# Performance work log

Measured on AMD Instinct MI355X. Metric: run time of the kernel, lower is better.

## Reference

```python
import jax, jax.numpy as jnp
import numpy as np

# ---- problem dims (match init_kwargs / input_specs) ----
MC = 2048        # max_concepts
D = 128          # embed_dim
B = 64           # batch
L = 16           # program length
NOBJ = 128       # objects per scene
FDIM = 512       # feature_dim
NN = MC + NOBJ   # num_nodes
TEMP = 3.0       # cosine temperature
TH = 0.8         # true_th (cosine, train==val)
POS = 10.0
NEG = -10.0
YES_IDX = 0      # protocol['concepts','yes']
NO_IDX = 1       # protocol['concepts','no']
INIT_VAR = 0.001


def setup_inputs() -> dict:
    key = jax.random.key(0)
    ks = jax.random.split(key, 6)
    scene = jax.random.normal(ks[0], (B, NOBJ, FDIM), jnp.float32)
    # program[:, :, 0] = op code in [0,7), program[:, :, 1] = argument index
    program = jax.random.randint(ks[1], (B, L, 2), 0, 7, dtype=jnp.int32)
    concept_table = jax.random.normal(ks[2], (MC, D), jnp.float32) * INIT_VAR
    relation_table = jax.random.normal(ks[3], (MC, D * D), jnp.float32) * INIT_VAR
    W_feat = jax.random.normal(ks[4], (FDIM, D), jnp.float32) * INIT_VAR
    b_feat = jax.random.normal(ks[5], (D,), jnp.float32) * INIT_VAR
    return {"scene": scene, "program": program, "concept_table": concept_table,
            "relation_table": relation_table, "W_feat": W_feat, "b_feat": b_feat}


def _cos_sim(x, y, eps=1e-8):
    # torch F.cosine_similarity semantics: clamp each norm at eps
    xn = jnp.maximum(jnp.linalg.norm(x, axis=-1), eps)
    yn = jnp.maximum(jnp.linalg.norm(y, axis=-1), eps)
    return jnp.sum(x * y, axis=-1) / (xn * yn)


def reference(scene, program, concept_table, relation_table, W_feat, b_feat):
    # feature_mlp (dim_hidden == 0 -> single Linear)
    objects = scene @ W_feat + b_feat                              # [B, NOBJ, D]
    # per-step embedded arguments
    concept_args = concept_table[program[:, :, 1]]                 # [B, L, D]
    rel_args = relation_table[program[:, :, 1]].reshape(B, L, D, D)
    node_is_concept = jnp.arange(NN) < MC                          # [NN]
    # all_nodes = concat(all_concepts, objects) per sample
    all_nodes = jnp.concatenate(
        [jnp.broadcast_to(concept_table[None], (B, MC, D)), objects], axis=1)  # [B, NN, D]

    def run_sample(nodes_i, ops_i, args_i, cargs_i, rargs_i):
        att0 = jnp.ones((NN,), jnp.float32)

        def body(att, inp):
            op, arg, cvec, rmat = inp

            def f_null(a):
                return a

            def f_sel_obj(a):  # select 'object_only': zero concept slots
                return jnp.where(node_is_concept, 0.0, a)

            def f_sel_con(a):  # select 'concept_only': zero object slots
                return jnp.where(node_is_concept, a, 0.0)

            def f_verify(a):
                sim = _cos_sim(nodes_i, cvec[None, :])             # [NN]
                return jnp.minimum(a, jax.nn.sigmoid((sim - TH) * TEMP))

            def f_choose(a):
                a = jnp.where(node_is_concept, 0.0, a)
                return a.at[arg].set(1.0)

            def f_exist(a):
                s = a.max()
                yes = s * POS
                no = POS - yes
                a = jnp.full_like(a, NEG)
                return a.at[YES_IDX].set(yes).at[NO_IDX].set(no)

            def f_transfer(a):
                gather = a @ nodes_i                               # [D]
                trans = gather @ rmat                              # [D]
                sim = _cos_sim(nodes_i, trans[None, :])            # [NN]
                return jax.nn.sigmoid((sim - TH) * TEMP) * a.max()

            new = jax.lax.switch(
                op, [f_null, f_sel_obj, f_sel_con, f_verify, f_choose,
                     f_exist, f_transfer], att)
            return new, new

        _, hist = jax.lax.scan(body, att0, (ops_i, args_i, cargs_i, rargs_i))
        return hist                                                # [L, NN]

    hist = jax.vmap(run_sample)(all_nodes, program[:, :, 0], program[:, :, 1],
                                concept_args, rel_args)            # [B, L, NN]
    attn_final = hist[:, -1, :MC]                                  # [B, MC]
    out = jax.nn.log_softmax(attn_final, axis=1)
    return out, hist
```

## Files before the change

kernel.cpp:

```cpp
#include <hip/hip_runtime.h>
#include <math.h>

#define MC   2048
#define DD   128
#define BB   64
#define LL   16
#define NOBJ 128
#define FDIM 512
#define NN   (MC + NOBJ)
#define TEMPC 3.0f
#define THC   0.8f
#define POSC  10.0f
#define NEGC  (-10.0f)
#define EPSC  1e-8f
#define NARG  8
#define NINF  (-3.402823466e38f)
#define NSCALE 256.0f

#define QB   4
#define PART (NN / QB)
#define TS   512
#define NEP  32

typedef unsigned short ushort_t;
typedef float v2f __attribute__((ext_vector_type(2)));

#if defined(__has_builtin)
#if __has_builtin(__builtin_amdgcn_cvt_pk_f32_fp8)
#define HAS_HW_FP8 1
#endif
#endif

__device__ __forceinline__ float e4m3_dec1(unsigned int bv) {
    unsigned int s = (bv >> 7) & 1u, E = (bv >> 3) & 15u, M = bv & 7u;
    float v;
    if (E) v = __uint_as_float(((E + 120u) << 23) | (M << 20));
    else   v = (float)M * 0.001953125f;
    return s ? -v : v;
}
__device__ __forceinline__ v2f f8pair_sw(unsigned int w) {
    v2f r; r[0] = e4m3_dec1(w & 0xffu); r[1] = e4m3_dec1((w >> 8) & 0xffu); return r;
}
#ifdef HAS_HW_FP8
#define F8LO(u) __builtin_amdgcn_cvt_pk_f32_fp8((u), false)
#define F8HI(u) __builtin_amdgcn_cvt_pk_f32_fp8((u), true)
#else
#define F8LO(u) f8pair_sw((u) & 0xffffu)
#define F8HI(u) f8pair_sw((u) >> 16)
#endif

__device__ __forceinline__ unsigned int f32_to_e4m3(float x) {
    float a = fabsf(x);
    unsigned int s = (__float_as_uint(x) >> 31) << 7;
    if (a == 0.0f) return s;
    if (a >= 448.0f) return s | 0x7Eu;
    int e; float m = frexpf(a, &e);
    if (e >= -5) {
        int mant = (int)rintf(m * 16.0f);
        if (mant == 16) { mant = 8; e++; if (e - 1 > 8) return s | 0x7Eu; }
        return s | ((unsigned)(e - 1 + 7) << 3) | (unsigned)(mant - 8);
    } else {
        int q = (int)rintf(a * 512.0f);
        if (q >= 8) return s | 0x08u;
        return s | (unsigned)q;
    }
}

#define DEC16(u, g) do { \
    v2f _p0 = F8LO((u).x), _p1 = F8HI((u).x), _p2 = F8LO((u).y), _p3 = F8HI((u).y); \
    v2f _p4 = F8LO((u).z), _p5 = F8HI((u).z), _p6 = F8LO((u).w), _p7 = F8HI((u).w); \
    g[0]=_p0[0]; g[1]=_p0[1]; g[2]=_p1[0];  g[3]=_p1[1]; \
    g[4]=_p2[0]; g[5]=_p2[1]; g[6]=_p3[0];  g[7]=_p3[1]; \
    g[8]=_p4[0]; g[9]=_p4[1]; g[10]=_p5[0]; g[11]=_p5[1]; \
    g[12]=_p6[0]; g[13]=_p6[1]; g[14]=_p7[0]; g[15]=_p7[1]; \
} while (0)

#define GEMB 256
#define CONB 512
#define SIGB 64

__global__ __launch_bounds__(256) void prep_all(
        const float* __restrict__ scene, const float* __restrict__ W,
        const float* __restrict__ bias, const float* __restrict__ ct,
        float* __restrict__ cnorm, float* __restrict__ onorm,
        unsigned char* __restrict__ ctf8, unsigned char* __restrict__ objf8,
        float* __restrict__ sigc, float* __restrict__ sigo,
        unsigned int* __restrict__ flags) {
    const int blk = blockIdx.x;
    const int tid = threadIdx.x;

    if (blk < GEMB) {
        __shared__ float sA[64][36];
        __shared__ float sB[64][132];
        __shared__ float cv[NARG][DD];
        __shared__ float cnn[NARG];
        const int b = blk >> 2, q3 = blk & 3;
        const int row0 = q3 * 32;
        if (blk == 0) {
            for (int i = tid; i < BB * NEP * QB; i += 256) flags[i] = 0u;
        }
        for (int i = tid; i < NARG * DD; i += 256) cv[i >> 7][i & 127] = ct[i];
        __syncthreads();
        if (tid < NARG) {
            float ss = 0.f;
            for (int i = 0; i < DD; i++) ss = fmaf(cv[tid][i], cv[tid][i], ss);
            cnn[tid] = fmaxf(sqrtf(ss), EPSC);
        }
        const int tx = tid & 31, ty = tid >> 5;
        float acc[4][4] = {{0.f,0.f,0.f,0.f},{0.f,0.f,0.f,0.f},{0.f,0.f,0.f,0.f},{0.f,0.f,0.f,0.f}};
        const float* sc = scene + ((size_t)b * NOBJ + row0) * FDIM;
        for (int k0 = 0; k0 < FDIM; k0 += 64) {
            {
                const int r = tid >> 3, kq = (tid & 7) * 8;
                const float* src = sc + (size_t)r * FDIM + k0 + kq;
                float4 v0 = *(const float4*)(src);
                float4 v1 = *(const float4*)(src + 4);
                sA[kq+0][r]=v0.x; sA[kq+1][r]=v0.y; sA[kq+2][r]=v0.z; sA[kq+3][r]=v0.w;
                sA[kq+4][r]=v1.x; sA[kq+5][r]=v1.y; sA[kq+6][r]=v1.z; sA[kq+7][r]=v1.w;
            }
            {
                const int kk = tid >> 2, colq = (tid & 3) * 32;
                const float* src = W + (size_t)(k0 + kk) * DD + colq;
                float4* dst = (float4*)&sB[kk][colq];
                #pragma unroll
                for (int j = 0; j < 8; j++) dst[j] = *(const float4*)(src + j * 4);
            }
            __syncthreads();
            #pragma unroll 8
            for (int kk = 0; kk < 64; kk++) {
                float4 a4 = *(const float4*)&sA[kk][ty * 4];
                float4 b4 = *(const float4*)&sB[kk][tx * 4];
                float av[4] = {a4.x, a4.y, a4.z, a4.w};
                float bv[4] = {b4.x, b4.y, b4.z, b4.w};
                #pragma unroll
                for (int i = 0; i < 4; i++)
                    #pragma unroll
                    for (int j = 0; j < 4; j++)
                        acc[i][j] = fmaf(av[i], bv[j], acc[i][j]);
            }
            __syncthreads();
        }
        {
            float4 bb4 = *(const float4*)(bias + tx * 4);
            float bv[4] = {bb4.x, bb4.y, bb4.z, bb4.w};
            #pragma unroll
            for (int i = 0; i < 4; i++)
                #pragma unroll
                for (int j = 0; j < 4; j++) acc[i][j] += bv[j];
        }
        float nrm4[4], inv4[4];
        #pragma unroll
        for (int i = 0; i < 4; i++) {
            float ss = 0.f;
            #pragma unroll
            for (int j = 0; j < 4; j++) ss = fmaf(acc[i][j], acc[i][j], ss);
            ss += __shfl_xor(ss, 1, 32);  ss += __shfl_xor(ss, 2, 32);
            ss += __shfl_xor(ss, 4, 32);  ss += __shfl_xor(ss, 8, 32);
            ss += __shfl_xor(ss, 16, 32);
            nrm4[i] = fmaxf(sqrtf(ss), EPSC);
            inv4[i] = NSCALE / nrm4[i];
        }
        const int grow = b * NOBJ + row0 + ty * 4;
        #pragma unroll
        for (int i = 0; i < 4; i++) {
            unsigned int w = f32_to_e4m3(acc[i][0] * inv4[i])
                           | (f32_to_e4m3(acc[i][1] * inv4[i]) << 8)
                           | (f32_to_e4m3(acc[i][2] * inv4[i]) << 16)
                           | (f32_to_e4m3(acc[i][3] * inv4[i]) << 24);
            *(unsigned int*)(objf8 + (size_t)(grow + i) * DD + tx * 4) = w;
        }
        if (tx == 0) {
            #pragma unroll
            for (int i = 0; i < 4; i++) onorm[grow + i] = nrm4[i];
        }
        #pragma unroll
        for (int a = 0; a < NARG; a++) {
            float dp[4];
            #pragma unroll
            for (int i = 0; i < 4; i++) {
                float d = 0.f;
                d = fmaf(acc[i][0], cv[a][tx*4+0], d);
                d = fmaf(acc[i][1], cv[a][tx*4+1], d);
                d = fmaf(acc[i][2], cv[a][tx*4+2], d);
                d = fmaf(acc[i][3], cv[a][tx*4+3], d);
                d += __shfl_xor(d, 1, 32);  d += __shfl_xor(d, 2, 32);
                d += __shfl_xor(d, 4, 32);  d += __shfl_xor(d, 8, 32);
                d += __shfl_xor(d, 16, 32);
                dp[i] = d;
            }
            if (tx == 0) {
                #pragma unroll
                for (int i = 0; i < 4; i++) {
                    float sim = dp[i] / (nrm4[i] * cnn[a]);
                    float g = 1.f / (1.f + __expf(-(sim - THC) * TEMPC));
                    sigo[((size_t)b * NARG + a) * NOBJ + row0 + ty * 4 + i] = g;
                }
            }
        }
        return;
    }

    if (blk < GEMB + CONB) {
        const int wid = tid >> 6, lane = tid & 63;
        const int r = (blk - GEMB) * 4 + wid;
        const float* row = ct + (size_t)r * DD;
        float2 xy = *(const float2*)(row + lane * 2);
        float ss = xy.x * xy.x + xy.y * xy.y;
        #pragma unroll
        for (int off = 32; off; off >>= 1) ss += __shfl_xor(ss, off, 64);
        float nrm = fmaxf(sqrtf(ss), EPSC);
        float inv = NSCALE / nrm;
        unsigned int b0 = f32_to_e4m3(xy.x * inv);
        unsigned int b1 = f32_to_e4m3(xy.y * inv);
        *(ushort_t*)(ctf8 + (size_t)r * DD + lane * 2) = (ushort_t)(b0 | (b1 << 8));
        if (lane == 0) cnorm[r] = nrm;
        return;
    }

    __shared__ float cv2[NARG][DD];
    __shared__ float cn2[NARG];
    for (int a = 0; a < NARG; a++)
        for (int i = tid; i < DD; i += 256) cv2[a][i] = ct[(size_t)a * DD + i];
    __syncthreads();
    if (tid < NARG) {
        float ss = 0.f;
        for (int i = 0; i < DD; i++) ss = fmaf(cv2[tid][i], cv2[tid][i], ss);
        cn2[tid] = fmaxf(sqrtf(ss), EPSC);
    }
    __syncthreads();
    const int sub = tid & 7, slot = tid >> 3;
    const int r = (blk - GEMB - CONB) * 32 + slot;
    const float* row = ct + (size_t)r * DD;
    float4 r0 = *(const float4*)(row + sub * 16 + 0);
    float4 r1 = *(const float4*)(row + sub * 16 + 4);
    float4 r2 = *(const float4*)(row + sub * 16 + 8);
    float4 r3 = *(const float4*)(row + sub * 16 + 12);
    float ssr = 0.f;
    ssr = fmaf(r0.x, r0.x, ssr); ssr = fmaf(r0.y, r0.y, ssr);
    ssr = fmaf(r0.z, r0.z, ssr); ssr = fmaf(r0.w, r0.w, ssr);
    ssr = fmaf(r1.x, r1.x, ssr); ssr = fmaf(r1.y, r1.y, ssr);
    ssr = fmaf(r1.z, r1.z, ssr); ssr = fmaf(r1.w, r1.w, ssr);
    ssr = fmaf(r2.x, r2.x, ssr); ssr = fmaf(r2.y, r2.y, ssr);
    ssr = fmaf(r2.z, r2.z, ssr); ssr = fmaf(r2.w, r2.w, ssr);
    ssr = fmaf(r3.x, r3.x, ssr); ssr = fmaf(r3.y, r3.y, ssr);
    ssr = fmaf(r3.z, r3.z, ssr); ssr = fmaf(r3.w, r3.w, ssr);
    ssr += __shfl_xor(ssr, 1, 64);
    ssr += __shfl_xor(ssr, 2, 64);
    ssr += __shfl_xor(ssr, 4, 64);
    float rn = fmaxf(sqrtf(ssr), EPSC);
    for (int a = 0; a < NARG; a++) {
        const float* c = &cv2[a][sub * 16];
        float dp = 0.f;
        dp = fmaf(r0.x, c[0], dp);  dp = fmaf(r0.y, c[1], dp);
        dp = fmaf(r0.z, c[2], dp);  dp = fmaf(r0.w, c[3], dp);
        dp = fmaf(r1.x, c[4], dp);  dp = fmaf(r1.y, c[5], dp);
        dp = fmaf(r1.z, c[6], dp);  dp = fmaf(r1.w, c[7], dp);
        dp = fmaf(r2.x, c[8], dp);  dp = fmaf(r2.y, c[9], dp);
        dp = fmaf(r2.z, c[10], dp); dp = fmaf(r2.w, c[11], dp);
        dp = fmaf(r3.x, c[12], dp); dp = fmaf(r3.y, c[13], dp);
        dp = fmaf(r3.z, c[14], dp); dp = fmaf(r3.w, c[15], dp);
        dp += __shfl_xor(dp, 1, 64);
        dp += __shfl_xor(dp, 2, 64);
        dp += __shfl_xor(dp, 4, 64);
        if (sub == 0) {
            float sim = dp / (rn * cn2[a]);
            float g = 1.f / (1.f + __expf(-(sim - THC) * TEMPC));
            sigc[(size_t)a * MC + r] = g;
        }
    }
}


#define GATH_ROW(row_) do { \
    const int _r = (row_); \
    uint4 _u = *(const uint4*)&nd[_r * DD + ((sub ^ (_r & 7)) << 4)]; \
    const float _a = att[_r] * nrmL[_r]; \
    float _g[16]; DEC16(_u, _g); \
    _Pragma("unroll") \
    for (int _j = 0; _j < 16; _j++) ac[_j] = fmaf(_a, _g[_j], ac[_j]); \
} while (0)

#define SIM_ROW(row_, COMB) do { \
    const int _r = (row_); \
    uint4 _u = *(const uint4*)&nd[_r * DD + ((sub ^ (_r & 7)) << 4)]; \
    float _g[16]; DEC16(_u, _g); \
    float _dp = 0.f; \
    _Pragma("unroll") \
    for (int _j = 0; _j < 16; _j++) _dp = fmaf(_g[_j], vv[_j], _dp); \
    _dp += __shfl_xor(_dp, 1, 64); \
    _dp += __shfl_xor(_dp, 2, 64); \
    _dp += __shfl_xor(_dp, 4, 64); \
    if (sub == 0) { \
        const float _sim = _dp * invden; \
        const float sg = 1.f / (1.f + __expf(-(_sim - THC) * TEMPC)); \
        COMB; \
    } \
} while (0)

#define AST(p, v) __hip_atomic_store((p), (v), __ATOMIC_RELAXED, __HIP_MEMORY_SCOPE_AGENT)
#define ALD(p)    __hip_atomic_load((p), __ATOMIC_RELAXED, __HIP_MEMORY_SCOPE_AGENT)

#define QBARRIER() do { \
    __syncthreads(); \
    if (tid == 0) { \
        unsigned int* _fl = myflag + (int)epoch * QB; \
        AST(&_fl[q], 1u); \
        unsigned _s; \
        do { _s = ALD(&_fl[0]) + ALD(&_fl[1]) + ALD(&_fl[2]) + ALD(&_fl[3]); } while (_s < 4u); \
    } \
    __syncthreads(); \
} while (0)

__global__ __launch_bounds__(TS) void scan_exec(
        const float* __restrict__ ct, const float* __restrict__ rt,
        const int* __restrict__ program,
        const float* __restrict__ cnorm, const float* __restrict__ onorm,
        const float* __restrict__ sigc, const float* __restrict__ sigo,
        const unsigned char* __restrict__ ctf8, const unsigned char* __restrict__ objf8,
        float* __restrict__ gpart, unsigned int* __restrict__ flags,
        float* __restrict__ out, float* __restrict__ hist) {

    const int b    = blockIdx.x & (BB - 1);
    const int q    = blockIdx.x >> 6;
    const int base = q * PART;
    const int tid  = threadIdx.x;
    const int lane = tid & 63, wid = tid >> 6;
    const int rg   = tid >> 3, sub = tid & 7;

    __shared__ __align__(16) unsigned char nd[PART * DD];
    __shared__ __align__(16) float att[PART];
    __shared__ __align__(16) float nrmL[PART];
    __shared__ __align__(16) float vec[DD];
    __shared__ __align__(16) float gvf[DD];
    __shared__ __align__(16) float part[8 * DD];
    __shared__ float wred[8];
    __shared__ float red2[8];
    __shared__ float s_sh;
    __shared__ float s_sh2;
    __shared__ int   sprog[2 * LL];

    const unsigned char* myobjf8 = objf8 + (size_t)b * NOBJ * DD;

    for (int idx = tid; idx < PART * 8; idx += TS) {
        const int row = idx >> 3, j = idx & 7;
        const int g   = base + row;
        const unsigned char* src = (g < MC) ? (ctf8 + (size_t)g * DD)
                                            : (myobjf8 + (size_t)(g - MC) * DD);
        uint4 v = *(const uint4*)(src + j * 16);
        *(uint4*)&nd[row * DD + ((j ^ (row & 7)) << 4)] = v;
    }
    for (int i = tid; i < PART; i += TS) {
        const int g = base + i;
        att[i]  = 1.0f;
        nrmL[i] = (g < MC) ? cnorm[g] : onorm[b * NOBJ + (g - MC)];
    }
    if (tid < 2 * LL) sprog[tid] = program[b * 2 * LL + tid];
    __syncthreads();

    unsigned int epoch = 0;
    float* gpb = gpart + (size_t)b * (2 * QB * 132);
    unsigned int* myflag = flags + b * (NEP * QB);

    for (int step = 0; step < LL; step++) {
        const int op  = sprog[2 * step];
        const int arg = sprog[2 * step + 1];
        float* hrow = hist + ((size_t)b * LL + step) * NN;

        if (op == 0) {
            for (int i = tid; i < PART; i += TS) hrow[base + i] = att[i];
        } else if (op == 1) {
            for (int i = tid; i < PART; i += TS) {
                const int g = base + i;
                const float nv = (g < MC) ? 0.0f : att[i];
                att[i] = nv; hrow[g] = nv;
            }
        } else if (op == 2) {
            for (int i = tid; i < PART; i += TS) {
                const int g = base + i;
                const float nv = (g < MC) ? att[i] : 0.0f;
                att[i] = nv; hrow[g] = nv;
            }
        } else if (op == 3 && arg < NARG) {
            const float* sc = sigc + (size_t)arg * MC;
            const float* so = sigo + ((size_t)b * NARG + arg) * NOBJ;
            for (int i = tid; i < PART; i += TS) {
                const int g = base + i;
                const float gg = (g < MC) ? sc[g] : so[g - MC];
                const float nv = fminf(att[i], gg);
                att[i] = nv; hrow[g] = nv;
            }
        } else if (op == 3) {
            __syncthreads();
            if (tid < DD) vec[tid] = ct[(size_t)arg * DD + tid];
            __syncthreads();
            const float cn = fmaxf(cnorm[arg], EPSC);
            const float invden = 1.0f / (NSCALE * cn);
            float vv[16];
            {
                const float4 v0 = *(const float4*)&vec[sub * 16 + 0];
                const float4 v1 = *(const float4*)&vec[sub * 16 + 4];
                const float4 v2 = *(const float4*)&vec[sub * 16 + 8];
                const float4 v3 = *(const float4*)&vec[sub * 16 + 12];
                vv[0]=v0.x; vv[1]=v0.y; vv[2]=v0.z; vv[3]=v0.w;
                vv[4]=v1.x; vv[5]=v1.y; vv[6]=v1.z; vv[7]=v1.w;
                vv[8]=v2.x; vv[9]=v2.y; vv[10]=v2.z; vv[11]=v2.w;
                vv[12]=v3.x; vv[13]=v3.y; vv[14]=v3.z; vv[15]=v3.w;
            }
            #pragma unroll
            for (int p = 0; p < 8; p++)
                SIM_ROW(rg + p * 64, { const float nv = fminf(att[_r], sg); att[_r] = nv; hrow[base + _r] = nv; });
            if (rg < PART - 512)
                SIM_ROW(rg + 512, { const float nv = fminf(att[_r], sg); att[_r] = nv; hrow[base + _r] = nv; });
            __syncthreads();
        } else if (op == 4) {
            for (int i = tid; i < PART; i += TS) {
                const int g = base + i;
                const float nv = (g < MC) ? ((g == arg) ? 1.0f : 0.0f) : att[i];
                att[i] = nv; hrow[g] = nv;
            }
        } else if (op == 5) {
            __syncthreads();
            float lm = NINF;
            for (int i = tid; i < PART; i += TS) lm = fmaxf(lm, att[i]);
            #pragma unroll
            for (int off = 32; off; off >>= 1) lm = fmaxf(lm, __shfl_xor(lm, off, 64));
            if (lane == 0) wred[wid] = lm;
            __syncthreads();
            epoch++;
            if (tid == 0) {
                float m = wred[0];
                #pragma unroll
                for (int w = 1; w < 8; w++) m = fmaxf(m, wred[w]);
                AST(&gpb[(size_t)((epoch & 1) * QB + q) * 132 + DD], m);
            }
            QBARRIER();
            if (tid == 0) {
                float* slotR = gpb + (size_t)((epoch & 1) * QB) * 132;
                float m = NINF;
                #pragma unroll
                for (int k = 0; k < QB; k++)
                    m = fmaxf(m, ALD(&slotR[k * 132 + DD]));
                s_sh = m;
            }
            __syncthreads();
            const float s = s_sh;
            const float yes = s * POSC, no = POSC - yes;
            for (int i = tid; i < PART; i += TS) {
                const int g = base + i;
                const float nv = (g == 0) ? yes : ((g == 1) ? no : NEGC);
                att[i] = nv; hrow[g] = nv;
            }
        } else if (op == 6) {
            __syncthreads();
            const float* rm = rt + (size_t)arg * (DD * DD);
            const int half = lane >> 5, dq = (lane & 31) * 4;
            float4 rmr[8];
            #pragma unroll
            for (int j = 0; j < 8; j++) {
                const int d = wid * 16 + half * 8 + j;
                rmr[j] = *(const float4*)(rm + (size_t)d * DD + dq);
            }
            float lm = NINF;
            for (int i = tid; i < PART; i += TS) lm = fmaxf(lm, att[i]);
            #pragma unroll
            for (int off = 32; off; off >>= 1) lm = fmaxf(lm, __shfl_xor(lm, off, 64));
            if (lane == 0) wred[wid] = lm;
            float ac[16];
            #pragma unroll
            for (int j = 0; j < 16; j++) ac[j] = 0.f;
            #pragma unroll
            for (int p = 0; p < 8; p++) GATH_ROW(rg + p * 64);
            if (rg < PART - 512) GATH_ROW(rg + 512);
            #pragma unroll
            for (int j = 0; j < 16; j++) {
                ac[j] += __shfl_xor(ac[j], 8, 64);
                ac[j] += __shfl_xor(ac[j], 16, 64);
                ac[j] += __shfl_xor(ac[j], 32, 64);
            }
            if (lane < 8) {
                float* dst = &part[wid * DD + lane * 16];
                #pragma unroll
                for (int k = 0; k < 4; k++)
                    *(float4*)(dst + k * 4) = make_float4(ac[k*4], ac[k*4+1], ac[k*4+2], ac[k*4+3]);
            }
            __syncthreads();
            epoch++;
            {
                float* slotW = gpb + (size_t)((epoch & 1) * QB + q) * 132;
                if (tid < DD) {
                    float gsum = 0.f;
                    #pragma unroll
                    for (int w = 0; w < 8; w++) gsum += part[w * DD + tid];
                    AST(&slotW[tid], gsum);
                }
                if (tid == DD) {
                    float m = wred[0];
                    #pragma unroll
                    for (int w = 1; w < 8; w++) m = fmaxf(m, wred[w]);
                    AST(&slotW[DD], m);
                }
            }
            QBARRIER();
            {
                float* slotR = gpb + (size_t)((epoch & 1) * QB) * 132;
                if (tid < DD) {
                    float gsum = 0.f;
                    #pragma unroll
                    for (int k = 0; k < QB; k++)
                        gsum += ALD(&slotR[k * 132 + tid]);
                    gvf[tid] = gsum;
                }
                if (tid == DD) {
                    float m = NINF;
                    #pragma unroll
                    for (int k = 0; k < QB; k++)
                        m = fmaxf(m, ALD(&slotR[k * 132 + DD]));
                    s_sh = m;
                }
            }
            __syncthreads();
            float qx = 0.f, qy = 0.f, qz = 0.f, qw = 0.f;
            #pragma unroll
            for (int j = 0; j < 8; j++) {
                const int d = wid * 16 + half * 8 + j;
                const float g = gvf[d];
                qx = fmaf(g, rmr[j].x, qx); qy = fmaf(g, rmr[j].y, qy);
                qz = fmaf(g, rmr[j].z, qz); qw = fmaf(g, rmr[j].w, qw);
            }
            qx += __shfl_xor(qx, 32, 64); qy += __shfl_xor(qy, 32, 64);
            qz += __shfl_xor(qz, 32, 64); qw += __shfl_xor(qw, 32, 64);
            if (lane < 32) *(float4*)&part[wid * DD + dq] = make_float4(qx, qy, qz, qw);
            __syncthreads();
            if (tid < DD) {
                float t = 0.f;
                #pragma unroll
                for (int w = 0; w < 8; w++) t += part[w * DD + tid];
                vec[tid] = t;
                float ss = t * t;
                #pragma unroll
                for (int off = 32; off; off >>= 1) ss += __shfl_xor(ss, off, 64);
                if (lane == 0) red2[wid] = ss;
            }
            __syncthreads();
            const float tn = fmaxf(sqrtf(red2[0] + red2[1]), EPSC * NSCALE);
            const float invden = 1.0f / (NSCALE * tn);
            const float s = s_sh;
            float vv[16];
            {
                const float4 v0 = *(const float4*)&vec[sub * 16 + 0];
                const float4 v1 = *(const float4*)&vec[sub * 16 + 4];
                const float4 v2 = *(const float4*)&vec[sub * 16 + 8];
                const float4 v3 = *(const float4*)&vec[sub * 16 + 12];
                vv[0]=v0.x; vv[1]=v0.y; vv[2]=v0.z; vv[3]=v0.w;
                vv[4]=v1.x; vv[5]=v1.y; vv[6]=v1.z; vv[7]=v1.w;
                vv[8]=v2.x; vv[9]=v2.y; vv[10]=v2.z; vv[11]=v2.w;
                vv[12]=v3.x; vv[13]=v3.y; vv[14]=v3.z; vv[15]=v3.w;
            }
            #pragma unroll
            for (int p = 0; p < 8; p++)
                SIM_ROW(rg + p * 64, { const float nv = sg * s; att[_r] = nv; hrow[base + _r] = nv; });
            if (rg < PART - 512)
                SIM_ROW(rg + 512, { const float nv = sg * s; att[_r] = nv; hrow[base + _r] = nv; });
            __syncthreads();
        }

        __syncthreads();
    }

    const int crows = (base + PART <= MC) ? PART : (MC - base);
    {
        float lm = NINF;
        for (int i = tid; i < crows; i += TS) lm = fmaxf(lm, att[i]);
        #pragma unroll
        for (int off = 32; off; off >>= 1) lm = fmaxf(lm, __shfl_xor(lm, off, 64));
        if (lane == 0) wred[wid] = lm;
    }
    __syncthreads();
    float mloc = wred[0];
    #pragma unroll
    for (int w = 1; w < 8; w++) mloc = fmaxf(mloc, wred[w]);
    {
        float lse = 0.f;
        for (int i = tid; i < crows; i += TS) lse += expf(att[i] - mloc);
        #pragma unroll
        for (int off = 32; off; off >>= 1) lse += __shfl_xor(lse, off, 64);
        if (lane == 0) red2[wid] = lse;
    }
    __syncthreads();
    epoch++;
    if (tid == 0) {
        float sloc = 0.f;
        #pragma unroll
        for (int w = 0; w < 8; w++) sloc += red2[w];
        float* slotW = gpb + (size_t)((epoch & 1) * QB + q) * 132;
        AST(&slotW[DD], mloc);
        AST(&slotW[DD + 1], sloc);
    }
    QBARRIER();
    if (tid == 0) {
        float* slotR = gpb + (size_t)((epoch & 1) * QB) * 132;
        float mg = NINF;
        float mq[QB], sq[QB];
        #pragma unroll
        for (int k = 0; k < QB; k++) {
            mq[k] = ALD(&slotR[k * 132 + DD]);
            sq[k] = ALD(&slotR[k * 132 + DD + 1]);
            mg = fmaxf(mg, mq[k]);
        }
        float se = 0.f;
        #pragma unroll
        for (int k = 0; k < QB; k++) se += sq[k] * expf(mq[k] - mg);
        s_sh  = mg;
        s_sh2 = logf(se);
    }
    __syncthreads();
    const float mglob = s_sh, ls = s_sh2;
    for (int i = tid; i < crows; i += TS)
        out[(size_t)b * MC + base + i] = att[i] - mglob - ls;
}

extern "C" void kernel_launch(void* const* d_in, const int* in_sizes, int n_in,
                              void* d_out, int out_size, void* d_ws, size_t ws_size,
                              hipStream_t stream) {
    const float* scene = (const float*)d_in[0];
    const int*   prog  = (const int*)d_in[1];
    const float* ct    = (const float*)d_in[2];
    const float* rt    = (const float*)d_in[3];
    const float* W     = (const float*)d_in[4];
    const float* bias  = (const float*)d_in[5];

    float* out  = (float*)d_out;
    float* hist = out + (size_t)BB * MC;

    float* cnorm = (float*)d_ws;
    float* onorm = cnorm + MC;
    float* sigc  = onorm + (size_t)BB * NOBJ;
    float* sigo  = sigc + (size_t)NARG * MC;
    float* gpart = sigo + (size_t)BB * NARG * NOBJ;
    unsigned int* flagbuf = (unsigned int*)(gpart + (size_t)BB * 2 * QB * 132);
    unsigned char* ctf8  = (unsigned char*)(flagbuf + BB * NEP * QB);
    unsigned char* objf8 = ctf8 + (size_t)MC * DD;

    prep_all<<<dim3(GEMB + CONB + SIGB), 256, 0, stream>>>(
        scene, W, bias, ct, cnorm, onorm, ctf8, objf8, sigc, sigo, flagbuf);
    scan_exec<<<dim3(BB * QB), TS, 0, stream>>>(ct, rt, prog, cnorm, onorm, sigc, sigo,
                                                ctf8, objf8, gpart, flagbuf, out, hist);
}
```

Measured before the change: 261.5 us.

## Fuse prep kernel into scan kernel, recomputing concept FP8/norms/sigmoids per block

Removes the separate prep_all launch and folds the object-feature GEMM, concept FP8 quantization, norms, and verify sigmoids into the scan kernel's prologue. Half the threads run the object GEMM while the other half quantize concept rows. Object data is exchanged across the four quarter-blocks of each sample through global memory and the existing flag barrier. The flag buffer is now cleared with a memset. This drops one kernel launch and the global round trip of precomputed concept data, but each of the 64 samples now recomputes the concept-table preprocessing redundantly. It also adds an extra inter-block barrier and raises shared-memory use per block.

```diff
diff --git a/kernel.cpp b/kernel.cpp
--- a/kernel.cpp
+++ b/kernel.cpp
@@ -21,6 +21,7 @@
 #define PART (NN / QB)
 #define TS   512
 #define NEP  32
+#define CTAIL 336
 
 typedef unsigned short ushort_t;
 typedef float v2f __attribute__((ext_vector_type(2)));
@@ -75,202 +76,6 @@
     g[12]=_p6[0]; g[13]=_p6[1]; g[14]=_p7[0]; g[15]=_p7[1]; \
 } while (0)
 
-#define GEMB 256
-#define CONB 512
-#define SIGB 64
-
-__global__ __launch_bounds__(256) void prep_all(
-        const float* __restrict__ scene, const float* __restrict__ W,
-        const float* __restrict__ bias, const float* __restrict__ ct,
-        float* __restrict__ cnorm, float* __restrict__ onorm,
-        unsigned char* __restrict__ ctf8, unsigned char* __restrict__ objf8,
-        float* __restrict__ sigc, float* __restrict__ sigo,
-        unsigned int* __restrict__ flags) {
-    const int blk = blockIdx.x;
-    const int tid = threadIdx.x;
-
-    if (blk < GEMB) {
-        __shared__ float sA[64][36];
-        __shared__ float sB[64][132];
-        __shared__ float cv[NARG][DD];
-        __shared__ float cnn[NARG];
-        const int b = blk >> 2, q3 = blk & 3;
-        const int row0 = q3 * 32;
-        if (blk == 0) {
-            for (int i = tid; i < BB * NEP * QB; i += 256) flags[i] = 0u;
-        }
-        for (int i = tid; i < NARG * DD; i += 256) cv[i >> 7][i & 127] = ct[i];
-        __syncthreads();
-        if (tid < NARG) {
-            float ss = 0.f;
-            for (int i = 0; i < DD; i++) ss = fmaf(cv[tid][i], cv[tid][i], ss);
-            cnn[tid] = fmaxf(sqrtf(ss), EPSC);
-        }
-        const int tx = tid & 31, ty = tid >> 5;
-        float acc[4][4] = {{0.f,0.f,0.f,0.f},{0.f,0.f,0.f,0.f},{0.f,0.f,0.f,0.f},{0.f,0.f,0.f,0.f}};
-        const float* sc = scene + ((size_t)b * NOBJ + row0) * FDIM;
-        for (int k0 = 0; k0 < FDIM; k0 += 64) {
-            {
-                const int r = tid >> 3, kq = (tid & 7) * 8;
-                const float* src = sc + (size_t)r * FDIM + k0 + kq;
-                float4 v0 = *(const float4*)(src);
-                float4 v1 = *(const float4*)(src + 4);
-                sA[kq+0][r]=v0.x; sA[kq+1][r]=v0.y; sA[kq+2][r]=v0.z; sA[kq+3][r]=v0.w;
-                sA[kq+4][r]=v1.x; sA[kq+5][r]=v1.y; sA[kq+6][r]=v1.z; sA[kq+7][r]=v1.w;
-            }
-            {
-                const int kk = tid >> 2, colq = (tid & 3) * 32;
-                const float* src = W + (size_t)(k0 + kk) * DD + colq;
-                float4* dst = (float4*)&sB[kk][colq];
-                #pragma unroll
-                for (int j = 0; j < 8; j++) dst[j] = *(const float4*)(src + j * 4);
-            }
-            __syncthreads();
-            #pragma unroll 8
-            for (int kk = 0; kk < 64; kk++) {
-                float4 a4 = *(const float4*)&sA[kk][ty * 4];
-                float4 b4 = *(const float4*)&sB[kk][tx * 4];
-                float av[4] = {a4.x, a4.y, a4.z, a4.w};
-                float bv[4] = {b4.x, b4.y, b4.z, b4.w};
-                #pragma unroll
-                for (int i = 0; i < 4; i++)
-                    #pragma unroll
-                    for (int j = 0; j < 4; j++)
-                        acc[i][j] = fmaf(av[i], bv[j], acc[i][j]);
-            }
-            __syncthreads();
-        }
-        {
-            float4 bb4 = *(const float4*)(bias + tx * 4);
-            float bv[4] = {bb4.x, bb4.y, bb4.z, bb4.w};
-            #pragma unroll
-            for (int i = 0; i < 4; i++)
-                #pragma unroll
-                for (int j = 0; j < 4; j++) acc[i][j] += bv[j];
-        }
-        float nrm4[4], inv4[4];
-        #pragma unroll
-        for (int i = 0; i < 4; i++) {
-            float ss = 0.f;
-            #pragma unroll
-            for (int j = 0; j < 4; j++) ss = fmaf(acc[i][j], acc[i][j], ss);
-            ss += __shfl_xor(ss, 1, 32);  ss += __shfl_xor(ss, 2, 32);
-            ss += __shfl_xor(ss, 4, 32);  ss += __shfl_xor(ss, 8, 32);
-            ss += __shfl_xor(ss, 16, 32);
-            nrm4[i] = fmaxf(sqrtf(ss), EPSC);
-            inv4[i] = NSCALE / nrm4[i];
-        }
-        const int grow = b * NOBJ + row0 + ty * 4;
-        #pragma unroll
-        for (int i = 0; i < 4; i++) {
-            unsigned int w = f32_to_e4m3(acc[i][0] * inv4[i])
-                           | (f32_to_e4m3(acc[i][1] * inv4[i]) << 8)
-                           | (f32_to_e4m3(acc[i][2] * inv4[i]) << 16)
-                           | (f32_to_e4m3(acc[i][3] * inv4[i]) << 24);
-            *(unsigned int*)(objf8 + (size_t)(grow + i) * DD + tx * 4) = w;
-        }
-        if (tx == 0) {
-            #pragma unroll
-            for (int i = 0; i < 4; i++) onorm[grow + i] = nrm4[i];
-        }
-        #pragma unroll
-        for (int a = 0; a < NARG; a++) {
-            float dp[4];
-            #pragma unroll
-            for (int i = 0; i < 4; i++) {
-                float d = 0.f;
-                d = fmaf(acc[i][0], cv[a][tx*4+0], d);
-                d = fmaf(acc[i][1], cv[a][tx*4+1], d);
-                d = fmaf(acc[i][2], cv[a][tx*4+2], d);
-                d = fmaf(acc[i][3], cv[a][tx*4+3], d);
-                d += __shfl_xor(d, 1, 32);  d += __shfl_xor(d, 2, 32);
-                d += __shfl_xor(d, 4, 32);  d += __shfl_xor(d, 8, 32);
-                d += __shfl_xor(d, 16, 32);
-                dp[i] = d;
-            }
-            if (tx == 0) {
-                #pragma unroll
-                for (int i = 0; i < 4; i++) {
-                    float sim = dp[i] / (nrm4[i] * cnn[a]);
-                    float g = 1.f / (1.f + __expf(-(sim - THC) * TEMPC));
-                    sigo[((size_t)b * NARG + a) * NOBJ + row0 + ty * 4 + i] = g;
-                }
-            }
-        }
-        return;
-    }
-
-    if (blk < GEMB + CONB) {
-        const int wid = tid >> 6, lane = tid & 63;
-        const int r = (blk - GEMB) * 4 + wid;
-        const float* row = ct + (size_t)r * DD;
-        float2 xy = *(const float2*)(row + lane * 2);
-        float ss = xy.x * xy.x + xy.y * xy.y;
-        #pragma unroll
-        for (int off = 32; off; off >>= 1) ss += __shfl_xor(ss, off, 64);
-        float nrm = fmaxf(sqrtf(ss), EPSC);
-        float inv = NSCALE / nrm;
-        unsigned int b0 = f32_to_e4m3(xy.x * inv);
-        unsigned int b1 = f32_to_e4m3(xy.y * inv);
-        *(ushort_t*)(ctf8 + (size_t)r * DD + lane * 2) = (ushort_t)(b0 | (b1 << 8));
-        if (lane == 0) cnorm[r] = nrm;
-        return;
-    }
-
-    __shared__ float cv2[NARG][DD];
-    __shared__ float cn2[NARG];
-    for (int a = 0; a < NARG; a++)
-        for (int i = tid; i < DD; i += 256) cv2[a][i] = ct[(size_t)a * DD + i];
-    __syncthreads();
-    if (tid < NARG) {
-        float ss = 0.f;
-        for (int i = 0; i < DD; i++) ss = fmaf(cv2[tid][i], cv2[tid][i], ss);
-        cn2[tid] = fmaxf(sqrtf(ss), EPSC);
-    }
-    __syncthreads();
-    const int sub = tid & 7, slot = tid >> 3;
-    const int r = (blk - GEMB - CONB) * 32 + slot;
-    const float* row = ct + (size_t)r * DD;
-    float4 r0 = *(const float4*)(row + sub * 16 + 0);
-    float4 r1 = *(const float4*)(row + sub * 16 + 4);
-    float4 r2 = *(const float4*)(row + sub * 16 + 8);
-    float4 r3 = *(const float4*)(row + sub * 16 + 12);
-    float ssr = 0.f;
-    ssr = fmaf(r0.x, r0.x, ssr); ssr = fmaf(r0.y, r0.y, ssr);
-    ssr = fmaf(r0.z, r0.z, ssr); ssr = fmaf(r0.w, r0.w, ssr);
-    ssr = fmaf(r1.x, r1.x, ssr); ssr = fmaf(r1.y, r1.y, ssr);
-    ssr = fmaf(r1.z, r1.z, ssr); ssr = fmaf(r1.w, r1.w, ssr);
-    ssr = fmaf(r2.x, r2.x, ssr); ssr = fmaf(r2.y, r2.y, ssr);
-    ssr = fmaf(r2.z, r2.z, ssr); ssr = fmaf(r2.w, r2.w, ssr);
-    ssr = fmaf(r3.x, r3.x, ssr); ssr = fmaf(r3.y, r3.y, ssr);
-    ssr = fmaf(r3.z, r3.z, ssr); ssr = fmaf(r3.w, r3.w, ssr);
-    ssr += __shfl_xor(ssr, 1, 64);
-    ssr += __shfl_xor(ssr, 2, 64);
-    ssr += __shfl_xor(ssr, 4, 64);
-    float rn = fmaxf(sqrtf(ssr), EPSC);
-    for (int a = 0; a < NARG; a++) {
-        const float* c = &cv2[a][sub * 16];
-        float dp = 0.f;
-        dp = fmaf(r0.x, c[0], dp);  dp = fmaf(r0.y, c[1], dp);
-        dp = fmaf(r0.z, c[2], dp);  dp = fmaf(r0.w, c[3], dp);
-        dp = fmaf(r1.x, c[4], dp);  dp = fmaf(r1.y, c[5], dp);
-        dp = fmaf(r1.z, c[6], dp);  dp = fmaf(r1.w, c[7], dp);
-        dp = fmaf(r2.x, c[8], dp);  dp = fmaf(r2.y, c[9], dp);
-        dp = fmaf(r2.z, c[10], dp); dp = fmaf(r2.w, c[11], dp);
-        dp = fmaf(r3.x, c[12], dp); dp = fmaf(r3.y, c[13], dp);
-        dp = fmaf(r3.z, c[14], dp); dp = fmaf(r3.w, c[15], dp);
-        dp += __shfl_xor(dp, 1, 64);
-        dp += __shfl_xor(dp, 2, 64);
-        dp += __shfl_xor(dp, 4, 64);
-        if (sub == 0) {
-            float sim = dp / (rn * cn2[a]);
-            float g = 1.f / (1.f + __expf(-(sim - THC) * TEMPC));
-            sigc[(size_t)a * MC + r] = g;
-        }
-    }
-}
-
-
 #define GATH_ROW(row_) do { \
     const int _r = (row_); \
     uint4 _u = *(const uint4*)&nd[_r * DD + ((sub ^ (_r & 7)) << 4)]; \
@@ -303,7 +108,7 @@
 #define QBARRIER() do { \
     __syncthreads(); \
     if (tid == 0) { \
-        unsigned int* _fl = myflag + (int)epoch * QB; \
+        unsigned int* _fl = flags + b * (NEP * QB) + (int)epoch * QB; \
         AST(&_fl[q], 1u); \
         unsigned _s; \
         do { _s = ALD(&_fl[0]) + ALD(&_fl[1]) + ALD(&_fl[2]) + ALD(&_fl[3]); } while (_s < 4u); \
@@ -312,11 +117,11 @@
 } while (0)
 
 __global__ __launch_bounds__(TS) void scan_exec(
-        const float* __restrict__ ct, const float* __restrict__ rt,
-        const int* __restrict__ program,
-        const float* __restrict__ cnorm, const float* __restrict__ onorm,
-        const float* __restrict__ sigc, const float* __restrict__ sigo,
-        const unsigned char* __restrict__ ctf8, const unsigned char* __restrict__ objf8,
+        const float* __restrict__ scene, const float* __restrict__ W,
+        const float* __restrict__ bias, const float* __restrict__ ct,
+        const float* __restrict__ rt, const int* __restrict__ program,
+        float* __restrict__ onorm_g, float* __restrict__ sigo_g,
+        unsigned char* __restrict__ objf8,
         float* __restrict__ gpart, unsigned int* __restrict__ flags,
         float* __restrict__ out, float* __restrict__ hist) {
 
@@ -326,10 +131,12 @@
     const int tid  = threadIdx.x;
     const int lane = tid & 63, wid = tid >> 6;
     const int rg   = tid >> 3, sub = tid & 7;
+    const int ccount = (base + PART <= MC) ? PART : (MC - base);
 
     __shared__ __align__(16) unsigned char nd[PART * DD];
     __shared__ __align__(16) float att[PART];
     __shared__ __align__(16) float nrmL[PART];
+    __shared__ __align__(16) float sigL[NARG][PART];
     __shared__ __align__(16) float vec[DD];
     __shared__ __align__(16) float gvf[DD];
     __shared__ __align__(16) float part[8 * DD];
@@ -337,29 +144,189 @@
     __shared__ float red2[8];
     __shared__ float s_sh;
     __shared__ float s_sh2;
+    __shared__ float cnn[NARG];
     __shared__ int   sprog[2 * LL];
 
-    const unsigned char* myobjf8 = objf8 + (size_t)b * NOBJ * DD;
-
-    for (int idx = tid; idx < PART * 8; idx += TS) {
-        const int row = idx >> 3, j = idx & 7;
-        const int g   = base + row;
-        const unsigned char* src = (g < MC) ? (ctf8 + (size_t)g * DD)
-                                            : (myobjf8 + (size_t)(g - MC) * DD);
-        uint4 v = *(const uint4*)(src + j * 16);
-        *(uint4*)&nd[row * DD + ((j ^ (row & 7)) << 4)] = v;
-    }
-    for (int i = tid; i < PART; i += TS) {
-        const int g = base + i;
-        att[i]  = 1.0f;
-        nrmL[i] = (g < MC) ? cnorm[g] : onorm[b * NOBJ + (g - MC)];
-    }
+    float (*sA)[36]  = (float (*)[36])(&nd[0]);
+    float (*sB)[132] = (float (*)[132])(&nd[9216]);
+
+    auto stage_row = [&](const int r0, const int s8) {
+        const float* crow = ct + (size_t)(base + r0) * DD + s8 * 16;
+        const float4 c0 = *(const float4*)(crow + 0);
+        const float4 c1 = *(const float4*)(crow + 4);
+        const float4 c2 = *(const float4*)(crow + 8);
+        const float4 c3 = *(const float4*)(crow + 12);
+        float ss = 0.f;
+        ss = fmaf(c0.x,c0.x,ss); ss = fmaf(c0.y,c0.y,ss); ss = fmaf(c0.z,c0.z,ss); ss = fmaf(c0.w,c0.w,ss);
+        ss = fmaf(c1.x,c1.x,ss); ss = fmaf(c1.y,c1.y,ss); ss = fmaf(c1.z,c1.z,ss); ss = fmaf(c1.w,c1.w,ss);
+        ss = fmaf(c2.x,c2.x,ss); ss = fmaf(c2.y,c2.y,ss); ss = fmaf(c2.z,c2.z,ss); ss = fmaf(c2.w,c2.w,ss);
+        ss = fmaf(c3.x,c3.x,ss); ss = fmaf(c3.y,c3.y,ss); ss = fmaf(c3.z,c3.z,ss); ss = fmaf(c3.w,c3.w,ss);
+        ss += __shfl_xor(ss, 1, 64); ss += __shfl_xor(ss, 2, 64); ss += __shfl_xor(ss, 4, 64);
+        const float rn = fmaxf(sqrtf(ss), EPSC);
+        const float inv = NSCALE / rn;
+        unsigned int u0 = f32_to_e4m3(c0.x*inv) | (f32_to_e4m3(c0.y*inv)<<8)
+                        | (f32_to_e4m3(c0.z*inv)<<16) | (f32_to_e4m3(c0.w*inv)<<24);
+        unsigned int u1 = f32_to_e4m3(c1.x*inv) | (f32_to_e4m3(c1.y*inv)<<8)
+                        | (f32_to_e4m3(c1.z*inv)<<16) | (f32_to_e4m3(c1.w*inv)<<24);
+        unsigned int u2 = f32_to_e4m3(c2.x*inv) | (f32_to_e4m3(c2.y*inv)<<8)
+                        | (f32_to_e4m3(c2.z*inv)<<16) | (f32_to_e4m3(c2.w*inv)<<24);
+        unsigned int u3 = f32_to_e4m3(c3.x*inv) | (f32_to_e4m3(c3.y*inv)<<8)
+                        | (f32_to_e4m3(c3.z*inv)<<16) | (f32_to_e4m3(c3.w*inv)<<24);
+        *(uint4*)&nd[r0 * DD + ((s8 ^ (r0 & 7)) << 4)] = make_uint4(u0, u1, u2, u3);
+        if (s8 == 0) nrmL[r0] = rn;
+        #pragma unroll
+        for (int a = 0; a < NARG; a++) {
+            const float* c = &part[a * DD + s8 * 16];
+            float dp = 0.f;
+            dp = fmaf(c0.x,c[0],dp);  dp = fmaf(c0.y,c[1],dp);  dp = fmaf(c0.z,c[2],dp);  dp = fmaf(c0.w,c[3],dp);
+            dp = fmaf(c1.x,c[4],dp);  dp = fmaf(c1.y,c[5],dp);  dp = fmaf(c1.z,c[6],dp);  dp = fmaf(c1.w,c[7],dp);
+            dp = fmaf(c2.x,c[8],dp);  dp = fmaf(c2.y,c[9],dp);  dp = fmaf(c2.z,c[10],dp); dp = fmaf(c2.w,c[11],dp);
+            dp = fmaf(c3.x,c[12],dp); dp = fmaf(c3.y,c[13],dp); dp = fmaf(c3.z,c[14],dp); dp = fmaf(c3.w,c[15],dp);
+            dp += __shfl_xor(dp, 1, 64); dp += __shfl_xor(dp, 2, 64); dp += __shfl_xor(dp, 4, 64);
+            if (s8 == 0) {
+                const float sim = dp / (rn * cnn[a]);
+                sigL[a][r0] = 1.f / (1.f + __expf(-(sim - THC) * TEMPC));
+            }
+        }
+    };
+
+    for (int i = tid; i < NARG * DD; i += TS) part[i] = ct[i];
+    for (int i = tid; i < PART; i += TS) att[i] = 1.0f;
     if (tid < 2 * LL) sprog[tid] = program[b * 2 * LL + tid];
     __syncthreads();
-
-    unsigned int epoch = 0;
+    if (tid < NARG) {
+        float ss = 0.f;
+        for (int i = 0; i < DD; i++) ss = fmaf(part[tid * DD + i], part[tid * DD + i], ss);
+        cnn[tid] = fmaxf(sqrtf(ss), EPSC);
+    }
+
+    const int tx = tid & 31, ty = (tid & 255) >> 5;
+    float acc[4][4] = {{0.f,0.f,0.f,0.f},{0.f,0.f,0.f,0.f},{0.f,0.f,0.f,0.f},{0.f,0.f,0.f,0.f}};
+    const float* sc = scene + ((size_t)b * NOBJ + q * 32) * FDIM;
+    for (int k0 = 0; k0 < FDIM; k0 += 64) {
+        if (tid < 256) {
+            {
+                const int r = tid >> 3, kq = (tid & 7) * 8;
+                const float* src = sc + (size_t)r * FDIM + k0 + kq;
+                float4 v0 = *(const float4*)(src);
+                float4 v1 = *(const float4*)(src + 4);
+                sA[kq+0][r]=v0.x; sA[kq+1][r]=v0.y; sA[kq+2][r]=v0.z; sA[kq+3][r]=v0.w;
+                sA[kq+4][r]=v1.x; sA[kq+5][r]=v1.y; sA[kq+6][r]=v1.z; sA[kq+7][r]=v1.w;
+            }
+            {
+                const int kk = tid >> 2, colq = (tid & 3) * 32;
+                const float* src = W + (size_t)(k0 + kk) * DD + colq;
+                float4* dst = (float4*)&sB[kk][colq];
+                #pragma unroll
+                for (int j = 0; j < 8; j++) dst[j] = *(const float4*)(src + j * 4);
+            }
+        }
+        __syncthreads();
+        if (tid < 256) {
+            #pragma unroll 8
+            for (int kk = 0; kk < 64; kk++) {
+                float4 a4 = *(const float4*)&sA[kk][ty * 4];
+                float4 b4 = *(const float4*)&sB[kk][tx * 4];
+                float av[4] = {a4.x, a4.y, a4.z, a4.w};
+                float bv[4] = {b4.x, b4.y, b4.z, b4.w};
+                #pragma unroll
+                for (int i = 0; i < 4; i++)
+                    #pragma unroll
+                    for (int j = 0; j < 4; j++)
+                        acc[i][j] = fmaf(av[i], bv[j], acc[i][j]);
+            }
+        } else {
+            const int vt = tid - 256;
+            const int r0 = CTAIL + (k0 >> 6) * 32 + (vt >> 3);
+            if (r0 < ccount) stage_row(r0, vt & 7);
+        }
+        __syncthreads();
+    }
+
+    if (tid < 256) {
+        float4 bb4 = *(const float4*)(bias + tx * 4);
+        #pragma unroll
+        for (int i = 0; i < 4; i++) {
+            acc[i][0] += bb4.x; acc[i][1] += bb4.y; acc[i][2] += bb4.z; acc[i][3] += bb4.w;
+        }
+        float nrm4[4], inv4[4];
+        #pragma unroll
+        for (int i = 0; i < 4; i++) {
+            float ss = 0.f;
+            #pragma unroll
+            for (int j = 0; j < 4; j++) ss = fmaf(acc[i][j], acc[i][j], ss);
+            ss += __shfl_xor(ss, 1, 64);  ss += __shfl_xor(ss, 2, 64);
+            ss += __shfl_xor(ss, 4, 64);  ss += __shfl_xor(ss, 8, 64);
+            ss += __shfl_xor(ss, 16, 64);
+            nrm4[i] = fmaxf(sqrtf(ss), EPSC);
+            inv4[i] = NSCALE / nrm4[i];
+        }
+        const int grow = b * NOBJ + q * 32 + ty * 4;
+        #pragma unroll
+        for (int i = 0; i < 4; i++) {
+            unsigned int w = f32_to_e4m3(acc[i][0] * inv4[i])
+                           | (f32_to_e4m3(acc[i][1] * inv4[i]) << 8)
+                           | (f32_to_e4m3(acc[i][2] * inv4[i]) << 16)
+                           | (f32_to_e4m3(acc[i][3] * inv4[i]) << 24);
+            AST((unsigned int*)(objf8 + (size_t)(grow + i) * DD + tx * 4), w);
+        }
+        if (tx == 0) {
+            #pragma unroll
+            for (int i = 0; i < 4; i++) AST(&onorm_g[grow + i], nrm4[i]);
+        }
+        #pragma unroll
+        for (int a = 0; a < NARG; a++) {
+            float dp[4];
+            #pragma unroll
+            for (int i = 0; i < 4; i++) {
+                float d = 0.f;
+                d = fmaf(acc[i][0], part[a * DD + tx*4+0], d);
+                d = fmaf(acc[i][1], part[a * DD + tx*4+1], d);
+                d = fmaf(acc[i][2], part[a * DD + tx*4+2], d);
+                d = fmaf(acc[i][3], part[a * DD + tx*4+3], d);
+                d += __shfl_xor(d, 1, 64);  d += __shfl_xor(d, 2, 64);
+                d += __shfl_xor(d, 4, 64);  d += __shfl_xor(d, 8, 64);
+                d += __shfl_xor(d, 16, 64);
+                dp[i] = d;
+            }
+            if (tx == 0) {
+                #pragma unroll
+                for (int i = 0; i < 4; i++) {
+                    float sim = dp[i] / (nrm4[i] * cnn[a]);
+                    float g = 1.f / (1.f + __expf(-(sim - THC) * TEMPC));
+                    AST(&sigo_g[((size_t)b * NARG + a) * NOBJ + q * 32 + ty * 4 + i], g);
+                }
+            }
+        }
+    }
+
+    for (int r0 = tid >> 3; r0 < CTAIL; r0 += 64) stage_row(r0, sub);
+
+    unsigned int epoch = 1;
+    QBARRIER();
+
+    if (base + PART > MC) {
+        const int ob = MC - base;
+        for (int idx = tid; idx < NOBJ * 8; idx += TS) {
+            const int row = idx >> 3, j = idx & 7;
+            const unsigned int* src = (const unsigned int*)(objf8 + ((size_t)b * NOBJ + row) * DD + j * 16);
+            unsigned int w0 = ALD((unsigned int*)&src[0]);
+            unsigned int w1 = ALD((unsigned int*)&src[1]);
+            unsigned int w2 = ALD((unsigned int*)&src[2]);
+            unsigned int w3 = ALD((unsigned int*)&src[3]);
+            const int r0 = ob + row;
+            *(uint4*)&nd[r0 * DD + ((j ^ (r0 & 7)) << 4)] = make_uint4(w0, w1, w2, w3);
+        }
+        for (int i = tid; i < NOBJ; i += TS)
+            nrmL[ob + i] = ALD(&onorm_g[b * NOBJ + i]);
+        for (int idx = tid; idx < NARG * NOBJ; idx += TS) {
+            const int a = idx >> 7, oo = idx & 127;
+            sigL[a][ob + oo] = ALD(&sigo_g[((size_t)b * NARG + a) * NOBJ + oo]);
+        }
+    }
+    __syncthreads();
+
     float* gpb = gpart + (size_t)b * (2 * QB * 132);
-    unsigned int* myflag = flags + b * (NEP * QB);
 
     for (int step = 0; step < LL; step++) {
         const int op  = sprog[2 * step];
@@ -381,19 +348,22 @@
                 att[i] = nv; hrow[g] = nv;
             }
         } else if (op == 3 && arg < NARG) {
-            const float* sc = sigc + (size_t)arg * MC;
-            const float* so = sigo + ((size_t)b * NARG + arg) * NOBJ;
             for (int i = tid; i < PART; i += TS) {
-                const int g = base + i;
-                const float gg = (g < MC) ? sc[g] : so[g - MC];
-                const float nv = fminf(att[i], gg);
-                att[i] = nv; hrow[g] = nv;
+                const float nv = fminf(att[i], sigL[arg][i]);
+                att[i] = nv; hrow[base + i] = nv;
             }
         } else if (op == 3) {
             __syncthreads();
             if (tid < DD) vec[tid] = ct[(size_t)arg * DD + tid];
             __syncthreads();
-            const float cn = fmaxf(cnorm[arg], EPSC);
+            if (tid < DD) {
+                float t = vec[tid], ss = t * t;
+                #pragma unroll
+                for (int off = 32; off; off >>= 1) ss += __shfl_xor(ss, off, 64);
+                if (lane == 0) red2[wid] = ss;
+            }
+            __syncthreads();
+            const float cn = fmaxf(sqrtf(red2[0] + red2[1]), EPSC);
             const float invden = 1.0f / (NSCALE * cn);
             float vv[16];
             {
@@ -567,7 +537,7 @@
         __syncthreads();
     }
 
-    const int crows = (base + PART <= MC) ? PART : (MC - base);
+    const int crows = ccount;
     {
         float lm = NINF;
         for (int i = tid; i < crows; i += TS) lm = fmaxf(lm, att[i]);
@@ -632,17 +602,13 @@
     float* out  = (float*)d_out;
     float* hist = out + (size_t)BB * MC;
 
-    float* cnorm = (float*)d_ws;
-    float* onorm = cnorm + MC;
-    float* sigc  = onorm + (size_t)BB * NOBJ;
-    float* sigo  = sigc + (size_t)NARG * MC;
+    float* onorm = (float*)d_ws;
+    float* sigo  = onorm + (size_t)BB * NOBJ;
     float* gpart = sigo + (size_t)BB * NARG * NOBJ;
     unsigned int* flagbuf = (unsigned int*)(gpart + (size_t)BB * 2 * QB * 132);
-    unsigned char* ctf8  = (unsigned char*)(flagbuf + BB * NEP * QB);
-    unsigned char* objf8 = ctf8 + (size_t)MC * DD;
-
-    prep_all<<<dim3(GEMB + CONB + SIGB), 256, 0, stream>>>(
-        scene, W, bias, ct, cnorm, onorm, ctf8, objf8, sigc, sigo, flagbuf);
-    scan_exec<<<dim3(BB * QB), TS, 0, stream>>>(ct, rt, prog, cnorm, onorm, sigc, sigo,
-                                                ctf8, objf8, gpart, flagbuf, out, hist);
+    unsigned char* objf8 = (unsigned char*)(flagbuf + BB * NEP * QB);
+
+    hipMemsetAsync(flagbuf, 0, (size_t)BB * NEP * QB * sizeof(unsigned int), stream);
+    scan_exec<<<dim3(BB * QB), TS, 0, stream>>>(scene, W, bias, ct, rt, prog,
+                                                onorm, sigo, objf8, gpart, flagbuf, out, hist);
 }
```

After: 315.8 us. +20.8%, slower.
